# Performance work log

Hardware: AMD Instinct MI355X
Metric: run time of the kernel (lower is better)

The kernel has to match this reference:

```python
import jax, jax.numpy as jnp
import numpy as np

N = 100000
E = 1600000
NFEAT = 256
NHID = 128


def setup_inputs() -> dict:
    key = jax.random.key(0)
    k1, k2, k3, k4 = jax.random.split(key, 4)
    x = jax.random.normal(k1, (N, NFEAT), dtype=jnp.float32)
    edge_index = jax.random.randint(k2, (2, E), 0, N, dtype=jnp.int64)
    # GCNConv linear weight (stored as [nfeat, nhid] so h = x @ W) + bias
    W = jax.random.normal(k3, (NFEAT, NHID), dtype=jnp.float32) / np.sqrt(NFEAT)
    b = jnp.zeros((NHID,), dtype=jnp.float32)
    # PReLU single shared slope parameter (torch default init 0.25)
    prelu_a = jnp.asarray(0.25, dtype=jnp.float32)
    return {"x": x, "edge_index": edge_index, "W": W, "b": b, "prelu_a": prelu_a}


def _gcn_prelu(x, edge_index, W, b, prelu_a):
    n = x.shape[0]
    # spectral_norm reparametrization: divide weight by its largest singular value
    sigma = jnp.linalg.norm(W.astype(jnp.float32), ord=2)
    h = x @ (W / sigma)  # [N, nhid]
    # add self-loops (PyG GCNConv default)
    loop = jnp.arange(n, dtype=edge_index.dtype)
    row = jnp.concatenate([edge_index[0], loop])  # source
    col = jnp.concatenate([edge_index[1], loop])  # destination
    # symmetric degree normalization: deg from destination counts
    deg = jax.ops.segment_sum(jnp.ones_like(col, dtype=h.dtype), col, num_segments=n)
    dinv = jnp.where(deg > 0, jax.lax.rsqrt(deg), 0.0)
    norm = dinv[row] * dinv[col]  # [E+N]
    msgs = h[row] * norm[:, None]  # [E+N, nhid] gather
    out = jax.ops.segment_sum(msgs, col, num_segments=n) + b  # scatter-add
    # PReLU with shared slope
    return jnp.where(out > 0, out, prelu_a * out)


def reference(x, edge_index, W, b, prelu_a):
    return _gcn_prelu(x, edge_index, W, b, prelu_a)
```

## Files before the change

### kernel.cpp

```cpp
#include <hip/hip_runtime.h>

#define NN 100000
#define EE 1600000
#define NF 256
#define NH 128

#define BK 98
#define BNODE 1024
#define CHUNK 4096
#define NCHUNK ((EE + CHUNK - 1) / CHUNK)
#define CAP 24576

typedef unsigned int u32;
typedef unsigned short u16;
typedef __attribute__((ext_vector_type(8))) short short8;
typedef __attribute__((ext_vector_type(4))) float f32x4;

static __device__ __forceinline__ u16 f2bf(float f) {
  u32 u = __float_as_uint(f);
  u32 r = (u + 0x7FFFu + ((u >> 16) & 1u)) >> 16;
  return (u16)r;
}
static __device__ __forceinline__ float bflo(u32 u) { return __uint_as_float(u << 16); }
static __device__ __forceinline__ float bfhi(u32 u) { return __uint_as_float(u & 0xFFFF0000u); }

__global__ __launch_bounds__(256) void k_p1s(const int* __restrict__ row,
                                             const int* __restrict__ col,
                                             u32* __restrict__ gcur,
                                             u32* __restrict__ binned,
                                             const float* __restrict__ W,
                                             u16* __restrict__ Wt2,
                                             float* __restrict__ sig) {
  __shared__ __align__(16) char SM[69632];
  int t = threadIdx.x;

  if (blockIdx.x < NCHUNK) {
    u32* keybuf = (u32*)SM;
    unsigned char* bktbuf = (unsigned char*)(SM + 16384);
    u32* hist = (u32*)(SM + 20480);
    u32* lstart = (u32*)(SM + 20992);
    u32* lofs = (u32*)(SM + 21504);
    u32* gb = (u32*)(SM + 22016);
    if (t < BK) hist[t] = 0;
    __syncthreads();
    int e0 = blockIdx.x * CHUNK;
    int n = min(CHUNK, EE - e0);
    for (int i = t; i < n; i += 256) {
      u32 d = (u32)col[e0 + i];
      atomicAdd(&hist[d >> 10], 1u);
    }
    __syncthreads();
    if (t == 0) {
      u32 s = 0;
      for (int b = 0; b < BK; b++) { lstart[b] = s; lofs[b] = s; s += hist[b]; }
    }
    __syncthreads();
    if (t < BK && hist[t]) gb[t] = (u32)t * CAP + atomicAdd(&gcur[t], hist[t]);
    __syncthreads();
    for (int i = t; i < n; i += 256) {
      u32 d = (u32)col[e0 + i];
      u32 s = (u32)row[e0 + i];
      u32 b = d >> 10;
      u32 p = atomicAdd(&lofs[b], 1u);
      keybuf[p] = ((d & 1023u) << 17) | s;
      bktbuf[p] = (unsigned char)b;
    }
    __syncthreads();
    for (int i = t; i < n; i += 256) {
      u32 b = bktbuf[i];
      binned[gb[b] + ((u32)i - lstart[b])] = keybuf[i];
    }
    return;
  }

  char* MB = SM;
  float* diag = (float*)(SM + 65536);
  float* red = (float*)(SM + 66048);
  float* uvec = (float*)(SM + 67072);
  int* jdx = (int*)(SM + 67584);
  float* itrS = (float*)(SM + 68096);
  int* jmS = (int*)(SM + 68100);
  int l = t & 63, w = t >> 6;
  int p = l & 15, q = l >> 4;

  for (int base = t * 4; base < NF * NH; base += 1024) {
    float4 v = *(const float4*)&W[base];
    int k = base >> 7, c0 = base & 127;
#pragma unroll
    for (int i = 0; i < 4; i++) {
      int c = c0 + i;
      int inner = (k * 2) ^ ((c & 7) << 4);
      *(u16*)(MB + c * 512 + inner) = f2bf(((const float*)&v)[i]);
    }
  }
  __syncthreads();
  for (int u = t; u < 16384; u += 256) {
    int h = u * 2;
    int n = h >> 12;
    int rem = h & 4095;
    int ks = rem >> 9;
    int rem2 = rem & 511;
    int ll = rem2 >> 3;
    int j = rem2 & 7;
    int c = n * 16 + (ll & 15);
    int k = ks * 32 + ((ll >> 4) << 3) + j;
    ((u32*)Wt2)[u] = *(u32*)(MB + c * 512 + ((2 * k) ^ ((c & 7) << 4)));
  }

  f32x4 acc[2][8] = {};
#pragma unroll
  for (int ks = 0; ks < 8; ks++) {
    int kb = (ks * 32 + q * 8) * 2;
    short8 afr[2], bfr[8];
#pragma unroll
    for (int m = 0; m < 2; m++) {
      int ra = w * 32 + m * 16 + p;
      afr[m] = *(const short8*)(MB + ra * 512 + (kb ^ ((ra & 7) << 4)));
    }
#pragma unroll
    for (int n = 0; n < 8; n++) {
      int r = n * 16 + p;
      bfr[n] = *(const short8*)(MB + r * 512 + (kb ^ ((r & 7) << 4)));
    }
#pragma unroll
    for (int m = 0; m < 2; m++)
#pragma unroll
      for (int n = 0; n < 8; n++)
        acc[m][n] = __builtin_amdgcn_mfma_f32_16x16x32_bf16(afr[m], bfr[n], acc[m][n], 0, 0, 0);
  }
#pragma unroll
  for (int m = 0; m < 2; m++)
#pragma unroll
    for (int n = 0; n < 8; n++)
#pragma unroll
      for (int g = 0; g < 4; g++) {
        int r = w * 32 + m * 16 + q * 4 + g;
        int c = n * 16 + p;
        if (r == c) diag[r] = acc[m][n][g];
      }
  __syncthreads();
  if (t < 128) red[t] = diag[t];
  __syncthreads();
  for (int d = 64; d > 0; d >>= 1) { if (t < d) red[t] += red[t + d]; __syncthreads(); }
  if (t == 0) itrS[0] = 1.0f / red[0];
  __syncthreads();
  {
    float itr = itrS[0];
#pragma unroll
    for (int m = 0; m < 2; m++)
#pragma unroll
      for (int n = 0; n < 8; n++)
#pragma unroll
        for (int g = 0; g < 4; g++) {
          int r = w * 32 + m * 16 + q * 4 + g;
          int c = n * 16 + p;
          *(u16*)(MB + r * 256 + ((c * 2) ^ ((r & 7) << 4))) = f2bf(acc[m][n][g] * itr);
        }
  }

  char* src = MB;
  char* dst = MB + 32768;
  for (int s = 0; s < 8; s++) {
    __syncthreads();
    f32x4 mac[2][8] = {};
#pragma unroll
    for (int ks = 0; ks < 4; ks++) {
      int kb = (ks * 32 + q * 8) * 2;
      short8 afr[2], bfr[8];
#pragma unroll
      for (int m = 0; m < 2; m++) {
        int ra = w * 32 + m * 16 + p;
        afr[m] = *(const short8*)(src + ra * 256 + (kb ^ ((ra & 7) << 4)));
      }
#pragma unroll
      for (int n = 0; n < 8; n++) {
        int r = n * 16 + p;
        bfr[n] = *(const short8*)(src + r * 256 + (kb ^ ((r & 7) << 4)));
      }
#pragma unroll
      for (int m = 0; m < 2; m++)
#pragma unroll
        for (int n = 0; n < 8; n++)
          mac[m][n] = __builtin_amdgcn_mfma_f32_16x16x32_bf16(afr[m], bfr[n], mac[m][n], 0, 0, 0);
    }
#pragma unroll
    for (int m = 0; m < 2; m++)
#pragma unroll
      for (int n = 0; n < 8; n++)
#pragma unroll
        for (int g = 0; g < 4; g++) {
          int r = w * 32 + m * 16 + q * 4 + g;
          int c = n * 16 + p;
          if (r == c) diag[r] = mac[m][n][g];
        }
    __syncthreads();
    if (t < 128) red[t] = diag[t];
    __syncthreads();
    for (int d = 64; d > 0; d >>= 1) { if (t < d) red[t] += red[t + d]; __syncthreads(); }
    if (t == 0) itrS[0] = 1.0f / red[0];
    __syncthreads();
    float it2 = itrS[0];
#pragma unroll
    for (int m = 0; m < 2; m++)
#pragma unroll
      for (int n = 0; n < 8; n++)
#pragma unroll
        for (int g = 0; g < 4; g++) {
          int r = w * 32 + m * 16 + q * 4 + g;
          int c = n * 16 + p;
          *(u16*)(dst + r * 256 + ((c * 2) ^ ((r & 7) << 4))) = f2bf(mac[m][n][g] * it2);
        }
    char* tmp = src; src = dst; dst = tmp;
  }
  __syncthreads();

  if (t < 128) { red[t] = diag[t]; jdx[t] = t; }
  __syncthreads();
  for (int d = 64; d > 0; d >>= 1) {
    if (t < d && red[t + d] > red[t]) { red[t] = red[t + d]; jdx[t] = jdx[t + d]; }
    __syncthreads();
  }
  if (t == 0) jmS[0] = jdx[0];
  __syncthreads();
  int jm = jmS[0];
  if (t < 128) {
    u16 hv = *(u16*)(src + jm * 256 + ((t * 2) ^ ((jm & 7) << 4)));
    uvec[t] = __uint_as_float(((u32)hv) << 16);
  }
  __syncthreads();
  {
    float a2 = 0.f;
    const float* wr = &W[t * NH];
    for (int k = 0; k < NH; k++) a2 += wr[k] * uvec[k];
    red[t] = a2 * a2;
  }
  __syncthreads();
  for (int d = 128; d > 0; d >>= 1) { if (t < d) red[t] += red[t + d]; __syncthreads(); }
  if (t == 0) itrS[0] = red[0];
  __syncthreads();
  float num = itrS[0];
  if (t < 128) red[t] = uvec[t] * uvec[t];
  __syncthreads();
  for (int d = 64; d > 0; d >>= 1) { if (t < d) red[t] += red[t + d]; __syncthreads(); }
  if (t == 0) sig[0] = rsqrtf(num / red[0]);
}

__global__ __launch_bounds__(1024) void k_p2(const u32* __restrict__ binned,
                                             const u32* __restrict__ gcur,
                                             uint2* __restrict__ offdeg,
                                             float* __restrict__ dinv,
                                             int* __restrict__ csr) {
  __shared__ u32 hist[BNODE];
  __shared__ u32 loff[BNODE];
  __shared__ u32 cur[BNODE];
  __shared__ u32 stage[CAP];
  int b = blockIdx.x, t = threadIdx.x;
  u32 base = (u32)b * CAP;
  u32 cnt = gcur[b];
  hist[t] = 0;
  __syncthreads();
  for (u32 i = t; i < cnt; i += BNODE) {
    u32 key = binned[base + i];
    atomicAdd(&hist[key >> 17], 1u);
  }
  __syncthreads();
  u32 v = hist[t];
  loff[t] = v;
  __syncthreads();
  for (int d = 1; d < BNODE; d <<= 1) {
    u32 x = loff[t];
    u32 y = (t >= d) ? loff[t - d] : 0u;
    __syncthreads();
    loff[t] = x + y;
    __syncthreads();
  }
  u32 ex = loff[t] - v;
  cur[t] = ex;
  int g = b * BNODE + t;
  if (g < NN) {
    offdeg[g] = make_uint2(base + ex, base + ex + v);
    dinv[g] = rsqrtf((float)(v + 1u));
  }
  __syncthreads();
  if (cnt <= CAP) {
    for (u32 i = t; i < cnt; i += BNODE) {
      u32 key = binned[base + i];
      u32 p = atomicAdd(&cur[key >> 17], 1u);
      stage[p] = key & 0x1FFFFu;
    }
    __syncthreads();
    for (u32 i = t; i < cnt; i += BNODE) csr[base + i] = (int)stage[i];
  } else {
    for (u32 i = t; i < cnt; i += BNODE) {
      u32 key = binned[base + i];
      u32 p = atomicAdd(&cur[key >> 17], 1u);
      csr[base + p] = (int)(key & 0x1FFFFu);
    }
  }
}

__global__ __launch_bounds__(256) void k_mfma(const float* __restrict__ x,
                                              const u16* __restrict__ Wt2,
                                              const float* __restrict__ dinv,
                                              u16* __restrict__ hs) {
  __shared__ __align__(16) char LB[65536];
  int t = threadIdx.x;
  int l = t & 63, w = t >> 6;
  int row0 = blockIdx.x * 128;
  int lr = l & 15;
  int lk = (l >> 4) * 8;

  const float4* x4 = (const float4*)x;
#pragma unroll 8
  for (int i = t; i < 128 * 64; i += 256) {
    int r = i >> 6;
    int cq = i & 63;
    int gr = row0 + r;
    if (gr >= NN) gr = NN - 1;
    float4 v = x4[(size_t)gr * 64 + cq];
    uint2 wv;
    wv.x = (u32)f2bf(v.x) | ((u32)f2bf(v.y) << 16);
    wv.y = (u32)f2bf(v.z) | ((u32)f2bf(v.w) << 16);
    int kb = cq * 8;
    *(uint2*)(LB + r * 512 + (kb ^ ((r & 7) << 4))) = wv;
  }
  __syncthreads();

  int rbase = w * 32;
  f32x4 acc[2][8] = {};
#pragma unroll
  for (int ks = 0; ks < 8; ks++) {
    short8 bfr[8];
#pragma unroll
    for (int n = 0; n < 8; n++)
      bfr[n] = *(const short8*)&Wt2[(size_t)(((n * 8 + ks) * 64) + l) * 8];
    short8 afr[2];
#pragma unroll
    for (int m = 0; m < 2; m++) {
      int r = rbase + m * 16 + lr;
      int kb = (ks * 32 + lk) * 2;
      afr[m] = *(const short8*)(LB + r * 512 + (kb ^ ((r & 7) << 4)));
    }
#pragma unroll
    for (int m = 0; m < 2; m++)
#pragma unroll
      for (int n = 0; n < 8; n++)
        acc[m][n] = __builtin_amdgcn_mfma_f32_16x16x32_bf16(afr[m], bfr[n], acc[m][n], 0, 0, 0);
  }

  __syncthreads();
  u16* tile = (u16*)LB;
#pragma unroll
  for (int m = 0; m < 2; m++) {
    int rbl = w * 32 + m * 16 + (l >> 4) * 4;
    float dv[4];
#pragma unroll
    for (int g = 0; g < 4; g++) {
      int r = row0 + rbl + g;
      dv[g] = (r < NN) ? dinv[r] : 0.f;
    }
#pragma unroll
    for (int n = 0; n < 8; n++)
#pragma unroll
      for (int g = 0; g < 4; g++)
        tile[(rbl + g) * 128 + n * 16 + lr] = f2bf(acc[m][n][g] * dv[g]);
  }
  __syncthreads();
  const uint4* tl = (const uint4*)tile;
  size_t outb = (size_t)row0 * NH;
#pragma unroll
  for (int k = 0; k < 8; k++) {
    int u = t + k * 256;
    if (row0 + (u >> 4) < NN) *(uint4*)&hs[outb + (size_t)u * 8] = tl[u];
  }
}

__global__ __launch_bounds__(256) void k_gather(const u16* __restrict__ hs,
                                                const int* __restrict__ csr,
                                                const uint2* __restrict__ offdeg,
                                                const float* __restrict__ dinv,
                                                const float* __restrict__ b,
                                                const float* __restrict__ pa,
                                                const float* __restrict__ sig,
                                                float* __restrict__ out) {
  int wid = threadIdx.x >> 6;
  int lane = threadIdx.x & 63;
  int n = blockIdx.x * 4 + wid;
  if (n >= NN) return;
  uint2 od = offdeg[n];
  u32 s0 = od.x, s1 = od.y;
  const u32* hrow = (const u32*)hs;
  float ax, ay;
  {
    u32 u = hrow[(size_t)n * 64 + lane];
    ax = bflo(u); ay = bfhi(u);
  }
  u32 e = s0;
  for (; e + 8 <= s1; e += 8) {
    int i0 = csr[e],     i1 = csr[e + 1], i2 = csr[e + 2], i3 = csr[e + 3];
    int i4 = csr[e + 4], i5 = csr[e + 5], i6 = csr[e + 6], i7 = csr[e + 7];
    u32 u0 = hrow[(size_t)i0 * 64 + lane];
    u32 u1 = hrow[(size_t)i1 * 64 + lane];
    u32 u2 = hrow[(size_t)i2 * 64 + lane];
    u32 u3 = hrow[(size_t)i3 * 64 + lane];
    u32 u4 = hrow[(size_t)i4 * 64 + lane];
    u32 u5 = hrow[(size_t)i5 * 64 + lane];
    u32 u6 = hrow[(size_t)i6 * 64 + lane];
    u32 u7 = hrow[(size_t)i7 * 64 + lane];
    ax += bflo(u0) + bflo(u1) + bflo(u2) + bflo(u3)
        + bflo(u4) + bflo(u5) + bflo(u6) + bflo(u7);
    ay += bfhi(u0) + bfhi(u1) + bfhi(u2) + bfhi(u3)
        + bfhi(u4) + bfhi(u5) + bfhi(u6) + bfhi(u7);
  }
  for (; e + 4 <= s1; e += 4) {
    int i0 = csr[e], i1 = csr[e + 1], i2 = csr[e + 2], i3 = csr[e + 3];
    u32 u0 = hrow[(size_t)i0 * 64 + lane];
    u32 u1 = hrow[(size_t)i1 * 64 + lane];
    u32 u2 = hrow[(size_t)i2 * 64 + lane];
    u32 u3 = hrow[(size_t)i3 * 64 + lane];
    ax += bflo(u0) + bflo(u1) + bflo(u2) + bflo(u3);
    ay += bfhi(u0) + bfhi(u1) + bfhi(u2) + bfhi(u3);
  }
  for (; e < s1; e++) {
    u32 u = hrow[(size_t)csr[e] * 64 + lane];
    ax += bflo(u); ay += bfhi(u);
  }
  float dv = dinv[n] * sig[0];
  float2 bb = *(const float2*)&b[lane * 2];
  float a = pa[0];
  float v0 = ax * dv + bb.x;
  float v1 = ay * dv + bb.y;
  float2 o;
  o.x = v0 > 0.f ? v0 : a * v0;
  o.y = v1 > 0.f ? v1 : a * v1;
  *(float2*)&out[(size_t)n * NH + lane * 2] = o;
}

extern "C" void kernel_launch(void* const* d_in, const int* in_sizes, int n_in,
                              void* d_out, int out_size, void* d_ws, size_t ws_size,
                              hipStream_t stream) {
  const float* x = (const float*)d_in[0];
  const int* ei = (const int*)d_in[1];
  const float* W = (const float*)d_in[2];
  const float* b = (const float*)d_in[3];
  const float* pa = (const float*)d_in[4];
  float* out = (float*)d_out;
  const int* row = ei;
  const int* col = ei + EE;

  char* base = (char*)d_ws;
  size_t o = 0;
  auto alloc = [&](size_t bytes) -> void* {
    void* p = base + o;
    o += (bytes + 63) & ~(size_t)63;
    return p;
  };
  u32* gcur = (u32*)alloc(BK * 4);
  float* sig = (float*)alloc(64);
  float* dinv = (float*)alloc((size_t)NN * 4);
  uint2* offdeg = (uint2*)alloc((size_t)NN * 8);
  u32* binned = (u32*)alloc((size_t)BK * CAP * 4);
  int* csr = (int*)alloc((size_t)BK * CAP * 4);
  u16* Wt2 = (u16*)alloc((size_t)NF * NH * 2);
  u16* hs = (u16*)alloc((size_t)NN * NH * 2);
  (void)ws_size; (void)in_sizes; (void)n_in; (void)out_size;

  hipMemsetAsync(gcur, 0, BK * 4, stream);
  k_p1s<<<NCHUNK + 1, 256, 0, stream>>>(row, col, gcur, binned, W, Wt2, sig);
  k_p2<<<BK, BNODE, 0, stream>>>(binned, gcur, offdeg, dinv, csr);
  k_mfma<<<(NN + 127) / 128, 256, 0, stream>>>(x, Wt2, dinv, hs);
  k_gather<<<(NN + 3) / 4, 256, 0, stream>>>(hs, csr, offdeg, dinv, b, pa, sig, out);
}
```

Baseline: 178.2 us.

## Move spectral-norm scratch matrices from LDS to global memory to shrink shared memory

The fused binning/spectral-norm kernel used a 68 KB static LDS array, mostly for the single spectral-norm block's W and Gram-matrix scratch. That limited how many binning blocks (NCHUNK of them) could share a CU. The scratch now lives in global buffers (Wtg, Mg0, Mg1) with threadfences, LDS drops to about 22 KB, and launch bounds request 4 blocks per CU. The cost is that the spectral-norm block's power iterations now go through global/L2 memory and run slower, which could lengthen the critical path if that block finishes last.

```diff
diff --git a/kernel.cpp b/kernel.cpp
--- a/kernel.cpp
+++ b/kernel.cpp
@@ -23,15 +23,19 @@
 }
 static __device__ __forceinline__ float bflo(u32 u) { return __uint_as_float(u << 16); }
 static __device__ __forceinline__ float bfhi(u32 u) { return __uint_as_float(u & 0xFFFF0000u); }
-
-__global__ __launch_bounds__(256) void k_p1s(const int* __restrict__ row,
-                                             const int* __restrict__ col,
-                                             u32* __restrict__ gcur,
-                                             u32* __restrict__ binned,
-                                             const float* __restrict__ W,
-                                             u16* __restrict__ Wt2,
-                                             float* __restrict__ sig) {
-  __shared__ __align__(16) char SM[69632];
+static __device__ __forceinline__ float bf2f(u16 h) { return __uint_as_float(((u32)h) << 16); }
+
+__global__ __launch_bounds__(256, 4) void k_p1s(const int* __restrict__ row,
+                                                const int* __restrict__ col,
+                                                u32* __restrict__ gcur,
+                                                u32* __restrict__ binned,
+                                                const float* __restrict__ W,
+                                                u16* __restrict__ Wt2,
+                                                u16* __restrict__ Wtg,
+                                                u16* __restrict__ Mg0,
+                                                u16* __restrict__ Mg1,
+                                                float* __restrict__ sig) {
+  __shared__ __align__(16) char SM[22784];
   int t = threadIdx.x;
 
   if (blockIdx.x < NCHUNK) {
@@ -73,27 +77,15 @@
     return;
   }
 
-  char* MB = SM;
-  float* diag = (float*)(SM + 65536);
-  float* red = (float*)(SM + 66048);
-  float* uvec = (float*)(SM + 67072);
-  int* jdx = (int*)(SM + 67584);
-  float* itrS = (float*)(SM + 68096);
-  int* jmS = (int*)(SM + 68100);
+  float* diag = (float*)SM;
+  float* red = (float*)(SM + 512);
+  float* uvec = (float*)(SM + 1536);
+  int* jdx = (int*)(SM + 2048);
+  float* itrS = (float*)(SM + 2560);
+  int* jmS = (int*)(SM + 2564);
   int l = t & 63, w = t >> 6;
   int p = l & 15, q = l >> 4;
 
-  for (int base = t * 4; base < NF * NH; base += 1024) {
-    float4 v = *(const float4*)&W[base];
-    int k = base >> 7, c0 = base & 127;
-#pragma unroll
-    for (int i = 0; i < 4; i++) {
-      int c = c0 + i;
-      int inner = (k * 2) ^ ((c & 7) << 4);
-      *(u16*)(MB + c * 512 + inner) = f2bf(((const float*)&v)[i]);
-    }
-  }
-  __syncthreads();
   for (int u = t; u < 16384; u += 256) {
     int h = u * 2;
     int n = h >> 12;
@@ -104,23 +96,31 @@
     int j = rem2 & 7;
     int c = n * 16 + (ll & 15);
     int k = ks * 32 + ((ll >> 4) << 3) + j;
-    ((u32*)Wt2)[u] = *(u32*)(MB + c * 512 + ((2 * k) ^ ((c & 7) << 4)));
-  }
+    u32 lo = f2bf(W[k * NH + c]);
+    u32 hi = f2bf(W[(k + 1) * NH + c]);
+    ((u32*)Wt2)[u] = lo | (hi << 16);
+  }
+  for (int idx = t; idx < NF * NH; idx += 256) {
+    int c = idx & 127, k = idx >> 7;
+    Wtg[c * 256 + k] = f2bf(W[k * NH + c]);
+  }
+  __threadfence();
+  __syncthreads();
 
   f32x4 acc[2][8] = {};
 #pragma unroll
   for (int ks = 0; ks < 8; ks++) {
-    int kb = (ks * 32 + q * 8) * 2;
+    int kb = ks * 32 + q * 8;
     short8 afr[2], bfr[8];
 #pragma unroll
     for (int m = 0; m < 2; m++) {
       int ra = w * 32 + m * 16 + p;
-      afr[m] = *(const short8*)(MB + ra * 512 + (kb ^ ((ra & 7) << 4)));
+      afr[m] = *(const short8*)&Wtg[ra * 256 + kb];
     }
 #pragma unroll
     for (int n = 0; n < 8; n++) {
       int r = n * 16 + p;
-      bfr[n] = *(const short8*)(MB + r * 512 + (kb ^ ((r & 7) << 4)));
+      bfr[n] = *(const short8*)&Wtg[r * 256 + kb];
     }
 #pragma unroll
     for (int m = 0; m < 2; m++)
@@ -154,28 +154,29 @@
         for (int g = 0; g < 4; g++) {
           int r = w * 32 + m * 16 + q * 4 + g;
           int c = n * 16 + p;
-          *(u16*)(MB + r * 256 + ((c * 2) ^ ((r & 7) << 4))) = f2bf(acc[m][n][g] * itr);
+          Mg0[r * 128 + c] = f2bf(acc[m][n][g] * itr);
         }
   }
-
-  char* src = MB;
-  char* dst = MB + 32768;
+  __threadfence();
+
+  u16* src = Mg0;
+  u16* dst = Mg1;
   for (int s = 0; s < 8; s++) {
     __syncthreads();
     f32x4 mac[2][8] = {};
 #pragma unroll
     for (int ks = 0; ks < 4; ks++) {
-      int kb = (ks * 32 + q * 8) * 2;
+      int kb = ks * 32 + q * 8;
       short8 afr[2], bfr[8];
 #pragma unroll
       for (int m = 0; m < 2; m++) {
         int ra = w * 32 + m * 16 + p;
-        afr[m] = *(const short8*)(src + ra * 256 + (kb ^ ((ra & 7) << 4)));
+        afr[m] = *(const short8*)&src[ra * 128 + kb];
       }
 #pragma unroll
       for (int n = 0; n < 8; n++) {
         int r = n * 16 + p;
-        bfr[n] = *(const short8*)(src + r * 256 + (kb ^ ((r & 7) << 4)));
+        bfr[n] = *(const short8*)&src[r * 128 + kb];
       }
 #pragma unroll
       for (int m = 0; m < 2; m++)
@@ -208,9 +209,10 @@
         for (int g = 0; g < 4; g++) {
           int r = w * 32 + m * 16 + q * 4 + g;
           int c = n * 16 + p;
-          *(u16*)(dst + r * 256 + ((c * 2) ^ ((r & 7) << 4))) = f2bf(mac[m][n][g] * it2);
+          dst[r * 128 + c] = f2bf(mac[m][n][g] * it2);
         }
-    char* tmp = src; src = dst; dst = tmp;
+    __threadfence();
+    u16* tmp = src; src = dst; dst = tmp;
   }
   __syncthreads();
 
@@ -223,10 +225,7 @@
   if (t == 0) jmS[0] = jdx[0];
   __syncthreads();
   int jm = jmS[0];
-  if (t < 128) {
-    u16 hv = *(u16*)(src + jm * 256 + ((t * 2) ^ ((jm & 7) << 4)));
-    uvec[t] = __uint_as_float(((u32)hv) << 16);
-  }
+  if (t < 128) uvec[t] = bf2f(src[jm * 128 + t]);
   __syncthreads();
   {
     float a2 = 0.f;
@@ -462,11 +461,15 @@
   u32* binned = (u32*)alloc((size_t)BK * CAP * 4);
   int* csr = (int*)alloc((size_t)BK * CAP * 4);
   u16* Wt2 = (u16*)alloc((size_t)NF * NH * 2);
+  u16* Wtg = (u16*)alloc((size_t)NF * NH * 2);
+  u16* Mg0 = (u16*)alloc((size_t)NH * NH * 2);
+  u16* Mg1 = (u16*)alloc((size_t)NH * NH * 2);
   u16* hs = (u16*)alloc((size_t)NN * NH * 2);
   (void)ws_size; (void)in_sizes; (void)n_in; (void)out_size;
 
   hipMemsetAsync(gcur, 0, BK * 4, stream);
-  k_p1s<<<NCHUNK + 1, 256, 0, stream>>>(row, col, gcur, binned, W, Wt2, sig);
+  k_p1s<<<NCHUNK + 1, 256, 0, stream>>>(row, col, gcur, binned, W, Wt2, Wtg,
+                                        Mg0, Mg1, sig);
   k_p2<<<BK, BNODE, 0, stream>>>(binned, gcur, offdeg, dinv, csr);
   k_mfma<<<(NN + 127) / 128, 256, 0, stream>>>(x, Wt2, dinv, hs);
   k_gather<<<(NN + 3) / 4, 256, 0, stream>>>(hs, csr, offdeg, dinv, b, pa, sig, out);
```

Result: slower. 247.1 us (+38.6%).
